# Kernel optimization log

Measured on AMD Instinct MI355X. Metric: run time of the kernel, lower is better.

Reference implementation:

```python
import jax, jax.numpy as jnp
import numpy as np

N_NODES = 100000
FEAT_DIM = 128
EMBED_DIM = 128
NUM_SAMPLE = 10


def setup_inputs() -> dict:
    key = jax.random.key(0)
    k1, k2, k3, k4, k5 = jax.random.split(key, 5)
    features = jax.random.normal(k1, (N_NODES, FEAT_DIM), dtype=jnp.float32)
    W1 = jax.random.normal(k2, (EMBED_DIM, FEAT_DIM), dtype=jnp.float32) * (1.0 / np.sqrt(FEAT_DIM))
    W2 = jax.random.normal(k3, (EMBED_DIM, EMBED_DIM), dtype=jnp.float32) * (1.0 / np.sqrt(EMBED_DIM))
    adj = jax.random.randint(k4, (N_NODES, NUM_SAMPLE), 0, N_NODES, dtype=jnp.int64)
    nodes = jax.random.randint(k5, (N_NODES,), 0, N_NODES, dtype=jnp.int64)
    return {"features": features, "W1": W1, "W2": W2, "adj": adj, "nodes": nodes}


def reference(features, W1, W2, adj, nodes):
    # 2-layer GraphSAGE with gcn=True: mean over {self} U sampled neighbors,
    # then relu(agg @ W.T). Layer 1 is computed for all nodes since layer 2
    # needs embeddings of arbitrary neighbors.
    n = features.shape[0]
    self_idx = jnp.arange(n, dtype=adj.dtype)[:, None]            # [N,1]
    neigh1 = jnp.concatenate([self_idx, adj], axis=1)             # [N,S+1]
    agg1 = jnp.mean(features[neigh1], axis=1)                     # [N,F] (gather+mean)
    h1 = jax.nn.relu(agg1 @ W1.T)                                 # [N,E]

    neigh2 = jnp.concatenate([nodes[:, None], adj[nodes]], axis=1)  # [B,S+1]
    agg2 = jnp.mean(h1[neigh2], axis=1)                           # [B,E]
    out = jax.nn.relu(agg2 @ W2.T).T                              # [E,B], Encoder returns embed_dim x num_nodes
    return out
```

## Files before the change

kernel.cpp:

```cpp
#include <hip/hip_runtime.h>

#define N_NODES 100000
#define DIM 128
#define NS 10
#define SCALE (1.0f / 11.0f)

typedef unsigned int uint;
typedef unsigned short ushort;
typedef __attribute__((ext_vector_type(8))) short bf16x8;
typedef __attribute__((ext_vector_type(4))) float f32x4;

__device__ inline float bl(uint u) {
    union { uint x; float f; } c; c.x = u << 16; return c.f;
}
__device__ inline uint f2b(float x) {
    union { float f; uint u; } c; c.f = x;
    return (c.u + 0x7FFFu + ((c.u >> 16) & 1u)) >> 16;
}

__global__ __launch_bounds__(256) void wsplit(const float* __restrict__ W1,
                                              const float* __restrict__ W2,
                                              ushort* __restrict__ o) {
    const int i = blockIdx.x * 256 + threadIdx.x;
    const float a = W1[i];
    uint h = f2b(a);
    o[i] = (ushort)h;
    o[16384 + i] = (ushort)f2b(a - bl(h));
    const float b = W2[i];
    h = f2b(b);
    o[32768 + i] = (ushort)h;
    o[49152 + i] = (ushort)f2b(b - bl(h));
}

__device__ inline void split8(const float4& a, const float4& b, bf16x8& h, bf16x8& l) {
    const float xs[8] = {a.x, a.y, a.z, a.w, b.x, b.y, b.z, b.w};
#pragma unroll
    for (int j = 0; j < 8; ++j) {
        const uint hb = f2b(xs[j]);
        h[j] = (short)hb;
        l[j] = (short)f2b(xs[j] - bl(hb));
    }
}

__global__ __launch_bounds__(256) void gemm1(const float* __restrict__ X,
                                             const ushort* __restrict__ Whi,
                                             const ushort* __restrict__ Wlo,
                                             ushort* __restrict__ C) {
    const int lane = threadIdx.x & 63;
    const int wave = threadIdx.x >> 6;
    const int m16 = lane & 15;
    const int kh = (lane >> 4) * 8;
    const int r0 = blockIdx.x * 32;
    const int ct0 = wave * 2;

    bf16x8 wh[2][4], wl[2][4];
#pragma unroll
    for (int c = 0; c < 2; ++c)
#pragma unroll
        for (int ks = 0; ks < 4; ++ks) {
            const size_t woff = (size_t)((ct0 + c) * 16 + m16) * DIM + ks * 32 + kh;
            wh[c][ks] = *reinterpret_cast<const bf16x8*>(Whi + woff);
            wl[c][ks] = *reinterpret_cast<const bf16x8*>(Wlo + woff);
        }

    f32x4 acc[2][2];
#pragma unroll
    for (int rt = 0; rt < 2; ++rt)
#pragma unroll
        for (int c = 0; c < 2; ++c) acc[rt][c] = (f32x4){0.f, 0.f, 0.f, 0.f};

    const float* ap0 = X + (size_t)(r0 + m16) * DIM + kh;
    const float* ap1 = ap0 + 16 * DIM;

#pragma unroll
    for (int ks = 0; ks < 4; ++ks) {
        const float4 x0a = *reinterpret_cast<const float4*>(ap0 + ks * 32);
        const float4 x0b = *reinterpret_cast<const float4*>(ap0 + ks * 32 + 4);
        const float4 x1a = *reinterpret_cast<const float4*>(ap1 + ks * 32);
        const float4 x1b = *reinterpret_cast<const float4*>(ap1 + ks * 32 + 4);
        bf16x8 ah[2], al[2];
        split8(x0a, x0b, ah[0], al[0]);
        split8(x1a, x1b, ah[1], al[1]);
#pragma unroll
        for (int c = 0; c < 2; ++c)
#pragma unroll
            for (int rt = 0; rt < 2; ++rt) {
                acc[rt][c] = __builtin_amdgcn_mfma_f32_16x16x32_bf16(ah[rt], wh[c][ks], acc[rt][c], 0, 0, 0);
                acc[rt][c] = __builtin_amdgcn_mfma_f32_16x16x32_bf16(al[rt], wh[c][ks], acc[rt][c], 0, 0, 0);
                acc[rt][c] = __builtin_amdgcn_mfma_f32_16x16x32_bf16(ah[rt], wl[c][ks], acc[rt][c], 0, 0, 0);
            }
    }

    const int rowadd = (lane >> 4) * 4;
#pragma unroll
    for (int rt = 0; rt < 2; ++rt)
#pragma unroll
        for (int r4 = 0; r4 < 4; ++r4) {
            const size_t row = r0 + rt * 16 + rowadd + r4;
#pragma unroll
            for (int c = 0; c < 2; ++c)
                C[row * DIM + (ct0 + c) * 16 + m16] = (ushort)f2b(acc[rt][c][r4]);
        }
}

__global__ __launch_bounds__(256) void gemm2t(const ushort* __restrict__ P,
                                              const ushort* __restrict__ Whi,
                                              const ushort* __restrict__ Wlo,
                                              float* __restrict__ out) {
    const int lane = threadIdx.x & 63;
    const int wave = threadIdx.x >> 6;
    const int m16 = lane & 15;
    const int kh = (lane >> 4) * 8;
    const int r0 = blockIdx.x * 32;
    const int ct0 = wave * 2;

    bf16x8 wh[2][4], wl[2][4];
#pragma unroll
    for (int c = 0; c < 2; ++c)
#pragma unroll
        for (int ks = 0; ks < 4; ++ks) {
            const size_t woff = (size_t)((ct0 + c) * 16 + m16) * DIM + ks * 32 + kh;
            wh[c][ks] = *reinterpret_cast<const bf16x8*>(Whi + woff);
            wl[c][ks] = *reinterpret_cast<const bf16x8*>(Wlo + woff);
        }

    f32x4 acc[2][2];
#pragma unroll
    for (int rt = 0; rt < 2; ++rt)
#pragma unroll
        for (int c = 0; c < 2; ++c) acc[rt][c] = (f32x4){0.f, 0.f, 0.f, 0.f};

    const ushort* ap0 = P + (size_t)(r0 + m16) * DIM + kh;
    const ushort* ap1 = ap0 + 16 * DIM;

#pragma unroll
    for (int ks = 0; ks < 4; ++ks) {
        const bf16x8 a0 = *reinterpret_cast<const bf16x8*>(ap0 + ks * 32);
        const bf16x8 a1 = *reinterpret_cast<const bf16x8*>(ap1 + ks * 32);
#pragma unroll
        for (int c = 0; c < 2; ++c) {
            acc[0][c] = __builtin_amdgcn_mfma_f32_16x16x32_bf16(a0, wh[c][ks], acc[0][c], 0, 0, 0);
            acc[0][c] = __builtin_amdgcn_mfma_f32_16x16x32_bf16(a0, wl[c][ks], acc[0][c], 0, 0, 0);
            acc[1][c] = __builtin_amdgcn_mfma_f32_16x16x32_bf16(a1, wh[c][ks], acc[1][c], 0, 0, 0);
            acc[1][c] = __builtin_amdgcn_mfma_f32_16x16x32_bf16(a1, wl[c][ks], acc[1][c], 0, 0, 0);
        }
    }

    const int rowadd = (lane >> 4) * 4;
#pragma unroll
    for (int rt = 0; rt < 2; ++rt)
#pragma unroll
        for (int c = 0; c < 2; ++c) {
            float4 v;
            v.x = fmaxf(acc[rt][c][0], 0.f);
            v.y = fmaxf(acc[rt][c][1], 0.f);
            v.z = fmaxf(acc[rt][c][2], 0.f);
            v.w = fmaxf(acc[rt][c][3], 0.f);
            const int e = (ct0 + c) * 16 + m16;
            const int b = r0 + rt * 16 + rowadd;
            *reinterpret_cast<float4*>(out + (size_t)e * N_NODES + b) = v;
        }
}

__global__ __launch_bounds__(256) void agg1(const ushort* __restrict__ FW,
                                            const int* __restrict__ adj,
                                            ushort* __restrict__ H) {
    const int t = threadIdx.x;
    const int team = t >> 5;
    const int j = t & 31;
    const int i = blockIdx.x * 8 + team;
    int av = 0;
    if (j < NS) av = adj[(size_t)i * NS + j];
    const uint* self = reinterpret_cast<const uint*>(FW + (size_t)i * DIM);
    const uint x = self[j], y = self[j + 32];
    float a0 = bl(x), a1 = bl(x >> 16), a2 = bl(y), a3 = bl(y >> 16);
#pragma unroll
    for (int s = 0; s < NS; ++s) {
        const int idx = __shfl(av, s, 32);
        const uint* rp = reinterpret_cast<const uint*>(FW + (size_t)idx * DIM);
        const uint u = rp[j], v = rp[j + 32];
        a0 += bl(u); a1 += bl(u >> 16); a2 += bl(v); a3 += bl(v >> 16);
    }
    a0 = fmaxf(a0 * SCALE, 0.f);
    a1 = fmaxf(a1 * SCALE, 0.f);
    a2 = fmaxf(a2 * SCALE, 0.f);
    a3 = fmaxf(a3 * SCALE, 0.f);
    uint* ph = reinterpret_cast<uint*>(H);
    ph[(size_t)i * 64 + j] = f2b(a0) | (f2b(a1) << 16);
    ph[(size_t)i * 64 + 32 + j] = f2b(a2) | (f2b(a3) << 16);
}

__global__ __launch_bounds__(256) void agg2b(const ushort* __restrict__ H,
                                             const int* __restrict__ adj,
                                             const int* __restrict__ nodes,
                                             ushort* __restrict__ P) {
    const int t = threadIdx.x;
    const int team = t >> 5;
    const int j = t & 31;
    const int i = blockIdx.x * 8 + team;
    const int n = nodes[i];
    int av = 0;
    if (j < NS) av = adj[(size_t)n * NS + j];
    const uint* self = reinterpret_cast<const uint*>(H + (size_t)n * DIM);
    const uint x = self[j], y = self[j + 32];
    float a0 = bl(x), a1 = bl(x >> 16), a2 = bl(y), a3 = bl(y >> 16);
#pragma unroll
    for (int s = 0; s < NS; ++s) {
        const int idx = __shfl(av, s, 32);
        const uint* rp = reinterpret_cast<const uint*>(H + (size_t)idx * DIM);
        const uint u = rp[j], v = rp[j + 32];
        a0 += bl(u); a1 += bl(u >> 16); a2 += bl(v); a3 += bl(v >> 16);
    }
    a0 *= SCALE; a1 *= SCALE; a2 *= SCALE; a3 *= SCALE;
    uint* pp = reinterpret_cast<uint*>(P);
    pp[(size_t)i * 64 + j] = f2b(a0) | (f2b(a1) << 16);
    pp[(size_t)i * 64 + 32 + j] = f2b(a2) | (f2b(a3) << 16);
}

extern "C" void kernel_launch(void* const* d_in, const int* in_sizes, int n_in,
                              void* d_out, int out_size, void* d_ws, size_t ws_size,
                              hipStream_t stream) {
    const float* features = (const float*)d_in[0];
    const float* W1 = (const float*)d_in[1];
    const float* W2 = (const float*)d_in[2];
    const int* adj = (const int*)d_in[3];
    const int* nodes = (const int*)d_in[4];
    float* out = (float*)d_out;

    const size_t NE = (size_t)N_NODES * DIM;
    ushort* fw = (ushort*)d_ws;
    ushort* h1 = fw + NE;
    ushort* wpl = h1 + NE;
    ushort* w1hi = wpl;
    ushort* w1lo = wpl + 16384;
    ushort* w2hi = wpl + 32768;
    ushort* w2lo = wpl + 49152;

    wsplit<<<64, 256, 0, stream>>>(W1, W2, wpl);
    gemm1<<<N_NODES / 32, 256, 0, stream>>>(features, w1hi, w1lo, fw);
    agg1<<<N_NODES / 8, 256, 0, stream>>>(fw, adj, h1);
    agg2b<<<N_NODES / 8, 256, 0, stream>>>(h1, adj, nodes, fw);
    gemm2t<<<N_NODES / 32, 256, 0, stream>>>(fw, w2hi, w2lo, out);
}
```

Baseline: 178.6 us.

## Stage GEMM activations through LDS, swap MFMA operands, vectorize aggregation loads

Both GEMM kernels now do cooperative loads of each block's 32-row activation tile into LDS in fragment order, split it to hi/lo bf16 once per element, and read MFMA fragments from LDS. gemm1 swaps the MFMA operand order so each lane holds four contiguous output columns, which allows packed 8-byte bf16 stores instead of scattered 2-byte stores. The aggregation kernels switch from two 4-byte loads per lane to one 8-byte uint2 load per lane, and do the same for stores. The aim is less redundant conversion work and better-coalesced global traffic, at the cost of an LDS round trip, a barrier, and an occupancy hint of 2.

```diff
diff --git a/kernel.cpp b/kernel.cpp
--- a/kernel.cpp
+++ b/kernel.cpp
@@ -32,134 +32,168 @@
     o[49152 + i] = (ushort)f2b(b - bl(h));
 }
 
-__device__ inline void split8(const float4& a, const float4& b, bf16x8& h, bf16x8& l) {
-    const float xs[8] = {a.x, a.y, a.z, a.w, b.x, b.y, b.z, b.w};
-#pragma unroll
-    for (int j = 0; j < 8; ++j) {
-        const uint hb = f2b(xs[j]);
-        h[j] = (short)hb;
-        l[j] = (short)f2b(xs[j] - bl(hb));
-    }
-}
-
-__global__ __launch_bounds__(256) void gemm1(const float* __restrict__ X,
-                                             const ushort* __restrict__ Whi,
-                                             const ushort* __restrict__ Wlo,
-                                             ushort* __restrict__ C) {
-    const int lane = threadIdx.x & 63;
-    const int wave = threadIdx.x >> 6;
+__global__ __launch_bounds__(256, 2) void gemm1(const float* __restrict__ X,
+                                                const ushort* __restrict__ Whi,
+                                                const ushort* __restrict__ Wlo,
+                                                ushort* __restrict__ C) {
+    __shared__ __align__(16) ushort lds[8192];
+    const int t = threadIdx.x;
+    const int lane = t & 63;
+    const int wave = t >> 6;
     const int m16 = lane & 15;
-    const int kh = (lane >> 4) * 8;
+    const int kq = lane >> 4;
     const int r0 = blockIdx.x * 32;
-    const int ct0 = wave * 2;
+
+    const int v0 = t, v1 = t + 256;
+    const int ln0 = v0 & 63, ln1 = v1 & 63;
+    const float* s0 = X + (size_t)(r0 + (v0 >> 8) * 16 + (ln0 & 15)) * DIM +
+                      ((v0 >> 6) & 3) * 32 + (ln0 >> 4) * 8;
+    const float* s1 = X + (size_t)(r0 + (v1 >> 8) * 16 + (ln1 & 15)) * DIM +
+                      ((v1 >> 6) & 3) * 32 + (ln1 >> 4) * 8;
+    const float4 f00 = *(const float4*)(s0);
+    const float4 f01 = *(const float4*)(s0 + 4);
+    const float4 f10 = *(const float4*)(s1);
+    const float4 f11 = *(const float4*)(s1 + 4);
 
     bf16x8 wh[2][4], wl[2][4];
 #pragma unroll
     for (int c = 0; c < 2; ++c)
 #pragma unroll
         for (int ks = 0; ks < 4; ++ks) {
-            const size_t woff = (size_t)((ct0 + c) * 16 + m16) * DIM + ks * 32 + kh;
-            wh[c][ks] = *reinterpret_cast<const bf16x8*>(Whi + woff);
-            wl[c][ks] = *reinterpret_cast<const bf16x8*>(Wlo + woff);
-        }
+            const size_t off = (size_t)((2 * wave + c) * 16 + m16) * DIM + ks * 32 + kq * 8;
+            wh[c][ks] = *(const bf16x8*)(Whi + off);
+            wl[c][ks] = *(const bf16x8*)(Wlo + off);
+        }
+
+    {
+        const float xs[8] = {f00.x, f00.y, f00.z, f00.w, f01.x, f01.y, f01.z, f01.w};
+        bf16x8 hi, lo;
+#pragma unroll
+        for (int j = 0; j < 8; ++j) {
+            const uint hb = f2b(xs[j]);
+            hi[j] = (short)hb;
+            lo[j] = (short)f2b(xs[j] - bl(hb));
+        }
+        *(bf16x8*)(lds + (v0 >> 6) * 512 + ln0 * 8) = hi;
+        *(bf16x8*)(lds + 4096 + (v0 >> 6) * 512 + ln0 * 8) = lo;
+    }
+    {
+        const float xs[8] = {f10.x, f10.y, f10.z, f10.w, f11.x, f11.y, f11.z, f11.w};
+        bf16x8 hi, lo;
+#pragma unroll
+        for (int j = 0; j < 8; ++j) {
+            const uint hb = f2b(xs[j]);
+            hi[j] = (short)hb;
+            lo[j] = (short)f2b(xs[j] - bl(hb));
+        }
+        *(bf16x8*)(lds + (v1 >> 6) * 512 + ln1 * 8) = hi;
+        *(bf16x8*)(lds + 4096 + (v1 >> 6) * 512 + ln1 * 8) = lo;
+    }
+    __syncthreads();
 
     f32x4 acc[2][2];
 #pragma unroll
-    for (int rt = 0; rt < 2; ++rt)
-#pragma unroll
-        for (int c = 0; c < 2; ++c) acc[rt][c] = (f32x4){0.f, 0.f, 0.f, 0.f};
-
-    const float* ap0 = X + (size_t)(r0 + m16) * DIM + kh;
-    const float* ap1 = ap0 + 16 * DIM;
+    for (int bt = 0; bt < 2; ++bt)
+#pragma unroll
+        for (int c = 0; c < 2; ++c) acc[bt][c] = (f32x4){0.f, 0.f, 0.f, 0.f};
 
 #pragma unroll
     for (int ks = 0; ks < 4; ++ks) {
-        const float4 x0a = *reinterpret_cast<const float4*>(ap0 + ks * 32);
-        const float4 x0b = *reinterpret_cast<const float4*>(ap0 + ks * 32 + 4);
-        const float4 x1a = *reinterpret_cast<const float4*>(ap1 + ks * 32);
-        const float4 x1b = *reinterpret_cast<const float4*>(ap1 + ks * 32 + 4);
-        bf16x8 ah[2], al[2];
-        split8(x0a, x0b, ah[0], al[0]);
-        split8(x1a, x1b, ah[1], al[1]);
-#pragma unroll
-        for (int c = 0; c < 2; ++c)
-#pragma unroll
-            for (int rt = 0; rt < 2; ++rt) {
-                acc[rt][c] = __builtin_amdgcn_mfma_f32_16x16x32_bf16(ah[rt], wh[c][ks], acc[rt][c], 0, 0, 0);
-                acc[rt][c] = __builtin_amdgcn_mfma_f32_16x16x32_bf16(al[rt], wh[c][ks], acc[rt][c], 0, 0, 0);
-                acc[rt][c] = __builtin_amdgcn_mfma_f32_16x16x32_bf16(ah[rt], wl[c][ks], acc[rt][c], 0, 0, 0);
+#pragma unroll
+        for (int bt = 0; bt < 2; ++bt) {
+            const int g = bt * 4 + ks;
+            const bf16x8 xh = *(const bf16x8*)(lds + g * 512 + lane * 8);
+            const bf16x8 xl = *(const bf16x8*)(lds + 4096 + g * 512 + lane * 8);
+#pragma unroll
+            for (int c = 0; c < 2; ++c) {
+                acc[bt][c] = __builtin_amdgcn_mfma_f32_16x16x32_bf16(wh[c][ks], xh, acc[bt][c], 0, 0, 0);
+                acc[bt][c] = __builtin_amdgcn_mfma_f32_16x16x32_bf16(wl[c][ks], xh, acc[bt][c], 0, 0, 0);
+                acc[bt][c] = __builtin_amdgcn_mfma_f32_16x16x32_bf16(wh[c][ks], xl, acc[bt][c], 0, 0, 0);
             }
-    }
-
-    const int rowadd = (lane >> 4) * 4;
-#pragma unroll
-    for (int rt = 0; rt < 2; ++rt)
-#pragma unroll
-        for (int r4 = 0; r4 < 4; ++r4) {
-            const size_t row = r0 + rt * 16 + rowadd + r4;
-#pragma unroll
-            for (int c = 0; c < 2; ++c)
-                C[row * DIM + (ct0 + c) * 16 + m16] = (ushort)f2b(acc[rt][c][r4]);
-        }
-}
-
-__global__ __launch_bounds__(256) void gemm2t(const ushort* __restrict__ P,
-                                              const ushort* __restrict__ Whi,
-                                              const ushort* __restrict__ Wlo,
-                                              float* __restrict__ out) {
-    const int lane = threadIdx.x & 63;
-    const int wave = threadIdx.x >> 6;
+        }
+    }
+
+#pragma unroll
+    for (int bt = 0; bt < 2; ++bt) {
+        const size_t row = (size_t)(r0 + bt * 16 + m16);
+#pragma unroll
+        for (int c = 0; c < 2; ++c) {
+            uint2 w;
+            w.x = f2b(acc[bt][c][0]) | (f2b(acc[bt][c][1]) << 16);
+            w.y = f2b(acc[bt][c][2]) | (f2b(acc[bt][c][3]) << 16);
+            *(uint2*)(C + row * DIM + (2 * wave + c) * 16 + kq * 4) = w;
+        }
+    }
+}
+
+__global__ __launch_bounds__(256, 2) void gemm2t(const ushort* __restrict__ P,
+                                                 const ushort* __restrict__ Whi,
+                                                 const ushort* __restrict__ Wlo,
+                                                 float* __restrict__ out) {
+    __shared__ __align__(16) ushort lds[4096];
+    const int t = threadIdx.x;
+    const int lane = t & 63;
+    const int wave = t >> 6;
     const int m16 = lane & 15;
-    const int kh = (lane >> 4) * 8;
+    const int kq = lane >> 4;
     const int r0 = blockIdx.x * 32;
-    const int ct0 = wave * 2;
+
+    const int v0 = t, v1 = t + 256;
+    const int ln0 = v0 & 63, ln1 = v1 & 63;
+    const ushort* s0 = P + (size_t)(r0 + (v0 >> 8) * 16 + (ln0 & 15)) * DIM +
+                       ((v0 >> 6) & 3) * 32 + (ln0 >> 4) * 8;
+    const ushort* s1 = P + (size_t)(r0 + (v1 >> 8) * 16 + (ln1 & 15)) * DIM +
+                       ((v1 >> 6) & 3) * 32 + (ln1 >> 4) * 8;
+    const bf16x8 p0 = *(const bf16x8*)(s0);
+    const bf16x8 p1 = *(const bf16x8*)(s1);
 
     bf16x8 wh[2][4], wl[2][4];
 #pragma unroll
     for (int c = 0; c < 2; ++c)
 #pragma unroll
         for (int ks = 0; ks < 4; ++ks) {
-            const size_t woff = (size_t)((ct0 + c) * 16 + m16) * DIM + ks * 32 + kh;
-            wh[c][ks] = *reinterpret_cast<const bf16x8*>(Whi + woff);
-            wl[c][ks] = *reinterpret_cast<const bf16x8*>(Wlo + woff);
-        }
+            const size_t off = (size_t)((2 * wave + c) * 16 + m16) * DIM + ks * 32 + kq * 8;
+            wh[c][ks] = *(const bf16x8*)(Whi + off);
+            wl[c][ks] = *(const bf16x8*)(Wlo + off);
+        }
+
+    *(bf16x8*)(lds + (v0 >> 6) * 512 + ln0 * 8) = p0;
+    *(bf16x8*)(lds + (v1 >> 6) * 512 + ln1 * 8) = p1;
+    __syncthreads();
 
     f32x4 acc[2][2];
 #pragma unroll
-    for (int rt = 0; rt < 2; ++rt)
-#pragma unroll
-        for (int c = 0; c < 2; ++c) acc[rt][c] = (f32x4){0.f, 0.f, 0.f, 0.f};
-
-    const ushort* ap0 = P + (size_t)(r0 + m16) * DIM + kh;
-    const ushort* ap1 = ap0 + 16 * DIM;
+    for (int bt = 0; bt < 2; ++bt)
+#pragma unroll
+        for (int c = 0; c < 2; ++c) acc[bt][c] = (f32x4){0.f, 0.f, 0.f, 0.f};
 
 #pragma unroll
     for (int ks = 0; ks < 4; ++ks) {
-        const bf16x8 a0 = *reinterpret_cast<const bf16x8*>(ap0 + ks * 32);
-        const bf16x8 a1 = *reinterpret_cast<const bf16x8*>(ap1 + ks * 32);
+#pragma unroll
+        for (int bt = 0; bt < 2; ++bt) {
+            const bf16x8 pa = *(const bf16x8*)(lds + (bt * 4 + ks) * 512 + lane * 8);
+#pragma unroll
+            for (int c = 0; c < 2; ++c) {
+                acc[bt][c] = __builtin_amdgcn_mfma_f32_16x16x32_bf16(pa, wh[c][ks], acc[bt][c], 0, 0, 0);
+                acc[bt][c] = __builtin_amdgcn_mfma_f32_16x16x32_bf16(pa, wl[c][ks], acc[bt][c], 0, 0, 0);
+            }
+        }
+    }
+
+#pragma unroll
+    for (int bt = 0; bt < 2; ++bt) {
+        const int b = r0 + bt * 16 + kq * 4;
 #pragma unroll
         for (int c = 0; c < 2; ++c) {
-            acc[0][c] = __builtin_amdgcn_mfma_f32_16x16x32_bf16(a0, wh[c][ks], acc[0][c], 0, 0, 0);
-            acc[0][c] = __builtin_amdgcn_mfma_f32_16x16x32_bf16(a0, wl[c][ks], acc[0][c], 0, 0, 0);
-            acc[1][c] = __builtin_amdgcn_mfma_f32_16x16x32_bf16(a1, wh[c][ks], acc[1][c], 0, 0, 0);
-            acc[1][c] = __builtin_amdgcn_mfma_f32_16x16x32_bf16(a1, wl[c][ks], acc[1][c], 0, 0, 0);
-        }
-    }
-
-    const int rowadd = (lane >> 4) * 4;
-#pragma unroll
-    for (int rt = 0; rt < 2; ++rt)
-#pragma unroll
-        for (int c = 0; c < 2; ++c) {
+            const int e = (2 * wave + c) * 16 + m16;
             float4 v;
-            v.x = fmaxf(acc[rt][c][0], 0.f);
-            v.y = fmaxf(acc[rt][c][1], 0.f);
-            v.z = fmaxf(acc[rt][c][2], 0.f);
-            v.w = fmaxf(acc[rt][c][3], 0.f);
-            const int e = (ct0 + c) * 16 + m16;
-            const int b = r0 + rt * 16 + rowadd;
-            *reinterpret_cast<float4*>(out + (size_t)e * N_NODES + b) = v;
-        }
+            v.x = fmaxf(acc[bt][c][0], 0.f);
+            v.y = fmaxf(acc[bt][c][1], 0.f);
+            v.z = fmaxf(acc[bt][c][2], 0.f);
+            v.w = fmaxf(acc[bt][c][3], 0.f);
+            *(float4*)(out + (size_t)e * N_NODES + b) = v;
+        }
+    }
 }
 
 __global__ __launch_bounds__(256) void agg1(const ushort* __restrict__ FW,
@@ -171,23 +205,22 @@
     const int i = blockIdx.x * 8 + team;
     int av = 0;
     if (j < NS) av = adj[(size_t)i * NS + j];
-    const uint* self = reinterpret_cast<const uint*>(FW + (size_t)i * DIM);
-    const uint x = self[j], y = self[j + 32];
-    float a0 = bl(x), a1 = bl(x >> 16), a2 = bl(y), a3 = bl(y >> 16);
+    const uint2 x = ((const uint2*)(FW + (size_t)i * DIM))[j];
+    float a0 = bl(x.x), a1 = bl(x.x >> 16), a2 = bl(x.y), a3 = bl(x.y >> 16);
 #pragma unroll
     for (int s = 0; s < NS; ++s) {
         const int idx = __shfl(av, s, 32);
-        const uint* rp = reinterpret_cast<const uint*>(FW + (size_t)idx * DIM);
-        const uint u = rp[j], v = rp[j + 32];
-        a0 += bl(u); a1 += bl(u >> 16); a2 += bl(v); a3 += bl(v >> 16);
+        const uint2 u = ((const uint2*)(FW + (size_t)idx * DIM))[j];
+        a0 += bl(u.x); a1 += bl(u.x >> 16); a2 += bl(u.y); a3 += bl(u.y >> 16);
     }
     a0 = fmaxf(a0 * SCALE, 0.f);
     a1 = fmaxf(a1 * SCALE, 0.f);
     a2 = fmaxf(a2 * SCALE, 0.f);
     a3 = fmaxf(a3 * SCALE, 0.f);
-    uint* ph = reinterpret_cast<uint*>(H);
-    ph[(size_t)i * 64 + j] = f2b(a0) | (f2b(a1) << 16);
-    ph[(size_t)i * 64 + 32 + j] = f2b(a2) | (f2b(a3) << 16);
+    uint2 w;
+    w.x = f2b(a0) | (f2b(a1) << 16);
+    w.y = f2b(a2) | (f2b(a3) << 16);
+    ((uint2*)(H + (size_t)i * DIM))[j] = w;
 }
 
 __global__ __launch_bounds__(256) void agg2b(const ushort* __restrict__ H,
@@ -201,20 +234,19 @@
     const int n = nodes[i];
     int av = 0;
     if (j < NS) av = adj[(size_t)n * NS + j];
-    const uint* self = reinterpret_cast<const uint*>(H + (size_t)n * DIM);
-    const uint x = self[j], y = self[j + 32];
-    float a0 = bl(x), a1 = bl(x >> 16), a2 = bl(y), a3 = bl(y >> 16);
+    const uint2 x = ((const uint2*)(H + (size_t)n * DIM))[j];
+    float a0 = bl(x.x), a1 = bl(x.x >> 16), a2 = bl(x.y), a3 = bl(x.y >> 16);
 #pragma unroll
     for (int s = 0; s < NS; ++s) {
         const int idx = __shfl(av, s, 32);
-        const uint* rp = reinterpret_cast<const uint*>(H + (size_t)idx * DIM);
-        const uint u = rp[j], v = rp[j + 32];
-        a0 += bl(u); a1 += bl(u >> 16); a2 += bl(v); a3 += bl(v >> 16);
+        const uint2 u = ((const uint2*)(H + (size_t)idx * DIM))[j];
+        a0 += bl(u.x); a1 += bl(u.x >> 16); a2 += bl(u.y); a3 += bl(u.y >> 16);
     }
     a0 *= SCALE; a1 *= SCALE; a2 *= SCALE; a3 *= SCALE;
-    uint* pp = reinterpret_cast<uint*>(P);
-    pp[(size_t)i * 64 + j] = f2b(a0) | (f2b(a1) << 16);
-    pp[(size_t)i * 64 + 32 + j] = f2b(a2) | (f2b(a3) << 16);
+    uint2 w;
+    w.x = f2b(a0) | (f2b(a1) << 16);
+    w.y = f2b(a2) | (f2b(a3) << 16);
+    ((uint2*)(P + (size_t)i * DIM))[j] = w;
 }
 
 extern "C" void kernel_launch(void* const* d_in, const int* in_sizes, int n_in,
```

Result: faster. 153.6 us (-14.0%).
